# Kernel tuning notes

Hardware: AMD Instinct MI355X
Metric: run time of the kernel (lower is better)

The kernel has to match this reference:

```python
import jax, jax.numpy as jnp
import numpy as np

B, S, D, H = 2, 2048, 1024, 16  # batch, seq_len, model dim, heads


def setup_inputs() -> dict:
    key = jax.random.key(0)
    ks = jax.random.split(key, 5)
    return {
        "x": jax.random.normal(ks[0], (B, S, D), jnp.float32),
        "idx": jax.random.randint(ks[1], (B,), 0, S),
        "weight": jnp.float32(0.5),
        "attn_forcing": 1,  # static python flag
        "w_qkv": jax.random.normal(ks[2], (D, 3 * D), jnp.float32) * 0.02,
        "b_qkv": jnp.zeros((3 * D,), jnp.float32),
        "w_proj": jax.random.normal(ks[3], (D, D), jnp.float32) * 0.02,
        "b_proj": jnp.zeros((D,), jnp.float32),
    }


def reference(x, idx, weight, attn_forcing, w_qkv, b_qkv, w_proj, b_proj):
    Bx, Sx, Dm = x.shape
    dh = Dm // H
    # qkv projection (Conv1D: x @ w + b)
    qkv = x @ w_qkv + b_qkv  # [B,S,3D]
    q, k, v = jnp.split(qkv, 3, axis=-1)
    q = q.reshape(Bx, Sx, H, dh).transpose(0, 2, 1, 3)  # [B,H,S,dh]
    k = k.reshape(Bx, Sx, H, dh).transpose(0, 2, 1, 3)
    v = v.reshape(Bx, Sx, H, dh).transpose(0, 2, 1, 3)
    alen = jnp.arange(Sx)
    mask = (alen[None, :] <= alen[:, None]).astype(x.dtype)  # [S,S] causal
    w = jnp.einsum('bhqd,bhkd->bhqk', q, k) / jnp.asarray(np.sqrt(dh), x.dtype)
    w = w * mask + jnp.asarray(-1e9, x.dtype) * (1 - mask)
    w = jax.nn.softmax(w, axis=-1)
    if attn_forcing:
        # post-softmax forcing reweight: positions >= idx scaled by weight, then renorm
        a = jnp.where(alen[None, :] >= idx[:, None], weight, jnp.asarray(1.0, x.dtype))  # [B,S]
        w = w * a[:, None, None, :]
        w = w / jnp.sum(w, axis=-1, keepdims=True)
    out = jnp.einsum('bhqk,bhkd->bhqd', w, v)  # [B,H,S,dh]
    out = out.transpose(0, 2, 1, 3).reshape(Bx, Sx, Dm)  # merge heads
    return out @ w_proj + b_proj
```

## Files before the change

### kernel.cpp

```cpp
#include <hip/hip_runtime.h>


typedef __attribute__((ext_vector_type(8))) short short8;
typedef __attribute__((ext_vector_type(4))) float f32x4;

#define MFMA_B16(a, b, c) __builtin_amdgcn_mfma_f32_16x16x32_bf16(a, b, c, 0, 0, 0)

#if __has_builtin(__builtin_amdgcn_exp2f)
#define EXP2(x) __builtin_amdgcn_exp2f(x)
#else
#define EXP2(x) exp2f(x)
#endif

static __device__ __forceinline__ unsigned short f2bf(float f) {
    union { float f; unsigned int u; } v;
    v.f = f;
    unsigned int r = (v.u + 0x7fffu + ((v.u >> 16) & 1u)) >> 16;
    return (unsigned short)r;
}

static __device__ __forceinline__ unsigned int pk_bf16(float a, float b) {
#if __has_builtin(__builtin_amdgcn_cvt_pk_bf16_f32)
    typedef __bf16 bf2 __attribute__((ext_vector_type(2)));
    union { bf2 v; unsigned int u; } c;
    c.v = __builtin_amdgcn_cvt_pk_bf16_f32(a, b);
    return c.u;
#else
    return (unsigned int)f2bf(a) | ((unsigned int)f2bf(b) << 16);
#endif
}

static __device__ __forceinline__ void gl_lds16(const void* g, void* l) {
    __builtin_amdgcn_global_load_lds(
        (const __attribute__((address_space(1))) unsigned int*)g,
        (__attribute__((address_space(3))) unsigned int*)l, 16, 0, 0);
}

__global__ __launch_bounds__(256) void convert_x_kernel(const float4* __restrict__ x,
                                                        ushort4* __restrict__ xb) {
    int i = blockIdx.x * 256 + threadIdx.x;
    float4 v = x[i];
    ushort4 o;
    o.x = f2bf(v.x); o.y = f2bf(v.y); o.z = f2bf(v.z); o.w = f2bf(v.w);
    xb[i] = o;
}

__global__ __launch_bounds__(256) void transpose_cvt_kernel(const float* __restrict__ in,
                                                            unsigned short* __restrict__ out,
                                                            int R, int C) {
    __shared__ float t[32][33];
    int c0 = blockIdx.x * 32, r0 = blockIdx.y * 32;
    int x = threadIdx.x, y = threadIdx.y;
    #pragma unroll
    for (int yy = y; yy < 32; yy += 8)
        t[yy][x] = in[(size_t)(r0 + yy) * C + (c0 + x)];
    __syncthreads();
    #pragma unroll
    for (int yy = y; yy < 32; yy += 8)
        out[(size_t)(c0 + yy) * R + (r0 + x)] = f2bf(t[x][yy]);
}

__global__ __launch_bounds__(256) void gemm_qkv_kernel(const unsigned short* __restrict__ A,
                                                       const unsigned short* __restrict__ Bt,
                                                       const float* __restrict__ bias,
                                                       unsigned short* __restrict__ q,
                                                       unsigned short* __restrict__ k,
                                                       unsigned short* __restrict__ vT) {
    __shared__ unsigned short As[128 * 64];
    __shared__ unsigned short Bs[128 * 64];
    const int tid = threadIdx.x;
    const int lane = tid & 63, wave = tid >> 6;
    const int l15 = lane & 15, quad = lane >> 4;
    const int wm = wave >> 1, wn = wave & 1;
    const int row0 = blockIdx.y * 128, col0 = blockIdx.x * 128;
    const int K = 1024;

    int srow[4], scol[4], sdst[4];
    #pragma unroll
    for (int h = 0; h < 4; ++h) {
        int D = h * 256 + wave * 64 + lane;
        srow[h] = D >> 3;
        scol[h] = ((D & 7) ^ (srow[h] & 7)) * 8;
        sdst[h] = (h * 256 + wave * 64) * 8;
    }

    f32x4 acc[4][4] = {};

    for (int kt = 0; kt < K; kt += 64) {
        #pragma unroll
        for (int h = 0; h < 4; ++h) {
            gl_lds16(&A[(size_t)(row0 + srow[h]) * K + kt + scol[h]], &As[sdst[h]]);
            gl_lds16(&Bt[(size_t)(col0 + srow[h]) * K + kt + scol[h]], &Bs[sdst[h]]);
        }
        __syncthreads();
        #pragma unroll
        for (int kk = 0; kk < 2; ++kk) {
            short8 af[4], bf[4];
            #pragma unroll
            for (int i = 0; i < 4; ++i) {
                int r = wm * 64 + i * 16 + l15;
                af[i] = *(const short8*)&As[r * 64 + (((kk * 4 + quad) ^ (r & 7)) * 8)];
            }
            #pragma unroll
            for (int j = 0; j < 4; ++j) {
                int r = wn * 64 + j * 16 + l15;
                bf[j] = *(const short8*)&Bs[r * 64 + (((kk * 4 + quad) ^ (r & 7)) * 8)];
            }
            #pragma unroll
            for (int i = 0; i < 4; ++i)
                #pragma unroll
                for (int j = 0; j < 4; ++j)
                    acc[i][j] = MFMA_B16(af[i], bf[j], acc[i][j]);
        }
        __syncthreads();
    }

    const int b = row0 >> 11;
    const int srow0 = row0 & 2047;

    if (blockIdx.x < 16) {
        #pragma unroll
        for (int i = 0; i < 4; ++i)
            #pragma unroll
            for (int j = 0; j < 4; ++j)
                #pragma unroll
                for (int r = 0; r < 4; ++r) {
                    int row = row0 + wm * 64 + i * 16 + quad * 4 + r;
                    int col = col0 + wn * 64 + j * 16 + l15;
                    float val = acc[i][j][r] + bias[col];
                    int which = col >> 10, rem = col & 1023;
                    int hh = rem >> 6, d = rem & 63;
                    int s = row & 2047;
                    size_t o = ((size_t)((b * 16 + hh) * 2048 + s)) * 64 + d;
                    if (which == 0) q[o] = f2bf(val * 0.1803368867f);
                    else k[o] = f2bf(val);
                }
    } else {
        unsigned short* tb = (wn == 0) ? As : Bs;
        #pragma unroll
        for (int i = 0; i < 4; ++i)
            #pragma unroll
            for (int j = 0; j < 4; ++j) {
                const int col6 = j * 16 + l15;
                const int gcol = col0 + wn * 64 + col6;
                const float bb = bias[gcol];
                const int chunk = wm * 8 + i * 2 + (quad >> 1);
                unsigned int* pw = (unsigned int*)&tb[col6 * 128 +
                    ((chunk ^ (col6 & 15)) * 8) + (quad & 1) * 4];
                pw[0] = pk_bf16(acc[i][j][0] + bb, acc[i][j][1] + bb);
                pw[1] = pk_bf16(acc[i][j][2] + bb, acc[i][j][3] + bb);
            }
        __syncthreads();
        const int c = tid >> 1;
        const int half = c >> 6, col6 = c & 63;
        const int rhalf = (tid & 1) * 64;
        const unsigned short* src = half ? Bs : As;
        const int hh = (blockIdx.x - 16) * 2 + half;
        unsigned short* dst = vT + ((size_t)((b * 16 + hh) * 64 + col6)) * 2048 + srow0 + rhalf;
        #pragma unroll
        for (int kk = 0; kk < 8; ++kk) {
            const int chunk = ((rhalf >> 3) + kk) ^ (col6 & 15);
            *(short8*)&dst[kk * 8] = *(const short8*)&src[col6 * 128 + chunk * 8];
        }
    }
}

__global__ __launch_bounds__(256) void gemm_proj_kernel(const unsigned short* __restrict__ A,
                                                        const unsigned short* __restrict__ Bt,
                                                        const float* __restrict__ bias,
                                                        float* __restrict__ out) {
    __shared__ unsigned short As[128 * 64];
    __shared__ unsigned short Bs[64 * 64];
    const int tid = threadIdx.x;
    const int lane = tid & 63, wave = tid >> 6;
    const int l15 = lane & 15, quad = lane >> 4;
    const int wm = wave >> 1, wn = wave & 1;
    const int row0 = blockIdx.y * 128, col0 = blockIdx.x * 64;
    const int K = 1024;

    int srow[4], scol[4], sdst[4];
    #pragma unroll
    for (int h = 0; h < 4; ++h) {
        int D = h * 256 + wave * 64 + lane;
        srow[h] = D >> 3;
        scol[h] = ((D & 7) ^ (srow[h] & 7)) * 8;
        sdst[h] = (h * 256 + wave * 64) * 8;
    }

    f32x4 acc[4][2] = {};

    for (int kt = 0; kt < K; kt += 64) {
        #pragma unroll
        for (int h = 0; h < 4; ++h)
            gl_lds16(&A[(size_t)(row0 + srow[h]) * K + kt + scol[h]], &As[sdst[h]]);
        #pragma unroll
        for (int h = 0; h < 2; ++h)
            gl_lds16(&Bt[(size_t)(col0 + srow[h]) * K + kt + scol[h]], &Bs[sdst[h]]);
        __syncthreads();
        #pragma unroll
        for (int kk = 0; kk < 2; ++kk) {
            short8 af[4], bf[2];
            #pragma unroll
            for (int i = 0; i < 4; ++i) {
                int r = wm * 64 + i * 16 + l15;
                af[i] = *(const short8*)&As[r * 64 + (((kk * 4 + quad) ^ (r & 7)) * 8)];
            }
            #pragma unroll
            for (int j = 0; j < 2; ++j) {
                int r = wn * 32 + j * 16 + l15;
                bf[j] = *(const short8*)&Bs[r * 64 + (((kk * 4 + quad) ^ (r & 7)) * 8)];
            }
            #pragma unroll
            for (int i = 0; i < 4; ++i)
                #pragma unroll
                for (int j = 0; j < 2; ++j)
                    acc[i][j] = MFMA_B16(af[i], bf[j], acc[i][j]);
        }
        __syncthreads();
    }

    #pragma unroll
    for (int i = 0; i < 4; ++i)
        #pragma unroll
        for (int j = 0; j < 2; ++j)
            #pragma unroll
            for (int r = 0; r < 4; ++r) {
                int row = row0 + wm * 64 + i * 16 + quad * 4 + r;
                int col = col0 + wn * 32 + j * 16 + l15;
                out[(size_t)row * 1024 + col] = acc[i][j][r] + bias[col];
            }
}

__global__ __launch_bounds__(256) void attn_kernel(const unsigned short* __restrict__ Q,
                                                   const unsigned short* __restrict__ Kg,
                                                   const unsigned short* __restrict__ Vt,
                                                   const int* __restrict__ idx,
                                                   const float* __restrict__ weight,
                                                   const int* __restrict__ forcing,
                                                   unsigned short* __restrict__ O) {
    __shared__ unsigned short Ks[2][4096];
    __shared__ unsigned short Vs[2][4096];
    __shared__ unsigned short Pw[4][1024];

    const int tid = threadIdx.x;
    const int lane = tid & 63, wave = tid >> 6;
    const int l15 = lane & 15, quad = lane >> 4;
    const int bid = blockIdx.x;
    const int u = bid >> 5, a = u & 7, qg = u >> 3;
    const int t = (qg == 0) ? (31 - a) : (qg == 1) ? (16 + a) : (qg == 2) ? (15 - a) : a;
    const int bh = bid & 31;
    const int b = bh >> 4, hh = bh & 15;
    const unsigned short* Qb = Q + (size_t)bh * 2048 * 64;
    const unsigned short* Kh = Kg + (size_t)bh * 2048 * 64;
    const unsigned short* Vh = Vt + (size_t)bh * 2048 * 64;

    const int idxb = idx[b];
    const float lw = (forcing[0] != 0) ? __log2f(weight[0]) : 0.0f;

    const int L0 = wave * 128 + lane;
    const int rS = L0 >> 3;
    const int cS = (L0 & 7) ^ (rS & 7);
    const int ldsOffJ0 = (wave * 128) * 8;
    const int ldsOffJ1 = (wave * 128 + 64) * 8;

    const int q0 = t * 64 + wave * 16;
    const int qrow = q0 + l15;

    short8 aq0 = *(const short8*)&Qb[(q0 + l15) * 64 + quad * 8];
    short8 aq1 = *(const short8*)&Qb[(q0 + l15) * 64 + 32 + quad * 8];

    const short8 ones8 = {0x3F80, 0x3F80, 0x3F80, 0x3F80, 0x3F80, 0x3F80, 0x3F80, 0x3F80};

    f32x4 o[4] = {};
    f32x4 lsum = {};

    const int nkb = t + 1;

    {
        const unsigned short* kg = Kh + (size_t)rS * 64 + cS * 8;
        const unsigned short* vg = Vh + (size_t)rS * 2048 + cS * 8;
        gl_lds16(kg,            &Ks[0][ldsOffJ0]);
        gl_lds16(kg + 8 * 64,   &Ks[0][ldsOffJ1]);
        gl_lds16(vg,            &Vs[0][ldsOffJ0]);
        gl_lds16(vg + 8 * 2048, &Vs[0][ldsOffJ1]);
    }
    __syncthreads();

    unsigned short* const pwb = &Pw[wave][0];
    const int pwr = l15 * 64;
    const int pa7 = l15 & 7;

    for (int kb = 0; kb < nkb; ++kb) {
        const int cur = kb & 1;
        const int kbase = kb * 64;
        if (kb + 1 < nkb) {
            const int nb = kbase + 64;
            const unsigned short* kg = Kh + (size_t)(nb + rS) * 64 + cS * 8;
            const unsigned short* vg = Vh + (size_t)rS * 2048 + nb + cS * 8;
            gl_lds16(kg,            &Ks[cur ^ 1][ldsOffJ0]);
            gl_lds16(kg + 8 * 64,   &Ks[cur ^ 1][ldsOffJ1]);
            gl_lds16(vg,            &Vs[cur ^ 1][ldsOffJ0]);
            gl_lds16(vg + 8 * 2048, &Vs[cur ^ 1][ldsOffJ1]);
        }

        const bool fullF = (kbase >= idxb);
        const bool bndF = (!fullF) && (kbase + 63 >= idxb);
        const float zu = fullF ? lw : 0.0f;

        f32x4 sT[4];
        #pragma unroll
        for (int kt = 0; kt < 4; ++kt) {
            const int row = kt * 16 + l15;
            short8 k0 = *(const short8*)&Ks[cur][row * 64 + ((quad ^ (row & 7)) * 8)];
            short8 k1 = *(const short8*)&Ks[cur][row * 64 + (((4 + quad) ^ (row & 7)) * 8)];
            f32x4 z;
            if (!bndF) {
                z[0] = zu; z[1] = zu; z[2] = zu; z[3] = zu;
            } else {
                #pragma unroll
                for (int r = 0; r < 4; ++r)
                    z[r] = (kbase + kt * 16 + quad * 4 + r >= idxb) ? lw : 0.0f;
            }
            z = MFMA_B16(k0, aq0, z);
            z = MFMA_B16(k1, aq1, z);
            sT[kt] = z;
        }

        if (kb == t) {
            #pragma unroll
            for (int kt = 0; kt < 4; ++kt)
                #pragma unroll
                for (int r = 0; r < 4; ++r)
                    if (kbase + kt * 16 + quad * 4 + r > qrow) sT[kt][r] = -3.0e38f;
        }

        #pragma unroll
        for (int kt = 0; kt < 4; ++kt)
            #pragma unroll
            for (int r = 0; r < 4; ++r)
                sT[kt][r] = EXP2(sT[kt][r]);

        #pragma unroll
        for (int kt = 0; kt < 4; ++kt) {
            unsigned int* pw = (unsigned int*)&pwb[pwr +
                (((kt * 2 + (quad >> 1)) ^ pa7) * 8) + (quad & 1) * 4];
            pw[0] = pk_bf16(sT[kt][0], sT[kt][1]);
            pw[1] = pk_bf16(sT[kt][2], sT[kt][3]);
        }

        short8 bp0 = *(const short8*)&pwb[pwr + ((quad ^ pa7) * 8)];
        short8 bp1 = *(const short8*)&pwb[pwr + (((4 + quad) ^ pa7) * 8)];

        lsum = MFMA_B16(ones8, bp0, lsum);
        lsum = MFMA_B16(ones8, bp1, lsum);

        #pragma unroll
        for (int dt = 0; dt < 4; ++dt) {
            const int row = dt * 16 + l15;
            short8 vf0 = *(const short8*)&Vs[cur][row * 64 + ((quad ^ (row & 7)) * 8)];
            short8 vf1 = *(const short8*)&Vs[cur][row * 64 + (((4 + quad) ^ (row & 7)) * 8)];
            f32x4 oo = o[dt];
            oo = MFMA_B16(vf0, bp0, oo);
            oo = MFMA_B16(vf1, bp1, oo);
            o[dt] = oo;
        }

        __syncthreads();
    }

    const float inv = 1.0f / lsum[0];
    unsigned short* sc = &Ks[0][0] + wave * 1152;
    #pragma unroll
    for (int dt = 0; dt < 4; ++dt)
        #pragma unroll
        for (int r = 0; r < 4; ++r)
            sc[l15 * 72 + dt * 16 + quad * 4 + r] = f2bf(o[dt][r] * inv);
    const size_t rowoff = ((size_t)(b * 2048 + q0 + l15)) * 1024 + hh * 64;
    #pragma unroll
    for (int h = 0; h < 2; ++h) {
        short8 v8 = *(const short8*)&sc[l15 * 72 + quad * 16 + h * 8];
        *(short8*)&O[rowoff + quad * 16 + h * 8] = v8;
    }
}

extern "C" void kernel_launch(void* const* d_in, const int* in_sizes, int n_in,
                              void* d_out, int out_size, void* d_ws, size_t ws_size,
                              hipStream_t stream) {
    const float* x        = (const float*)d_in[0];
    const int*   idx      = (const int*)d_in[1];
    const float* weight   = (const float*)d_in[2];
    const int*   forcing  = (const int*)d_in[3];
    const float* w_qkv    = (const float*)d_in[4];
    const float* b_qkv    = (const float*)d_in[5];
    const float* w_proj   = (const float*)d_in[6];
    const float* b_proj   = (const float*)d_in[7];
    float* out = (float*)d_out;

    char* ws = (char*)d_ws;
    unsigned short* xb      = (unsigned short*)(ws);
    unsigned short* wqkvT   = (unsigned short*)(ws + 8388608);
    unsigned short* wprojT  = (unsigned short*)(ws + 14680064);
    unsigned short* qbuf    = (unsigned short*)(ws + 16777216);
    unsigned short* kbuf    = (unsigned short*)(ws + 25165824);
    unsigned short* vTbuf   = (unsigned short*)(ws + 33554432);
    unsigned short* attn_out = xb;

    convert_x_kernel<<<4096, 256, 0, stream>>>((const float4*)x, (ushort4*)xb);
    transpose_cvt_kernel<<<dim3(96, 32), dim3(32, 8), 0, stream>>>(w_qkv, wqkvT, 1024, 3072);
    transpose_cvt_kernel<<<dim3(32, 32), dim3(32, 8), 0, stream>>>(w_proj, wprojT, 1024, 1024);
    gemm_qkv_kernel<<<dim3(24, 32), 256, 0, stream>>>(xb, wqkvT, b_qkv, qbuf, kbuf, vTbuf);
    attn_kernel<<<1024, 256, 0, stream>>>(qbuf, kbuf, vTbuf, idx, weight, forcing, attn_out);
    gemm_proj_kernel<<<dim3(16, 32), 256, 0, stream>>>(attn_out, wprojT, b_proj, out);
}
```

Measured before the change: 194.3 us.

## Merge prep kernels and swap MFMA operands for vectorized GEMM epilogues

Merges the x conversion and the two weight transpose-convert launches into one prep kernel. Swaps the MFMA operand order in the Q/K and projection GEMMs so each lane holds four consecutive output columns, which lets the epilogues write packed bf16 uint2 and float4 stores instead of scalar ones. The V epilogue no longer goes through an LDS transpose and writes transposed rows straight from registers. This trims launch overhead and uncoalesced scalar stores, but the direct V stores are 8-byte pieces that may coalesce less well than the old LDS-staged 16-byte writes.

Result: faster. 189.4 us (-2.5%).

```diff
diff --git a/kernel.cpp b/kernel.cpp
--- a/kernel.cpp
+++ b/kernel.cpp
@@ -36,28 +36,43 @@
         (__attribute__((address_space(3))) unsigned int*)l, 16, 0, 0);
 }
 
-__global__ __launch_bounds__(256) void convert_x_kernel(const float4* __restrict__ x,
-                                                        ushort4* __restrict__ xb) {
-    int i = blockIdx.x * 256 + threadIdx.x;
-    float4 v = x[i];
-    ushort4 o;
-    o.x = f2bf(v.x); o.y = f2bf(v.y); o.z = f2bf(v.z); o.w = f2bf(v.w);
-    xb[i] = o;
-}
-
-__global__ __launch_bounds__(256) void transpose_cvt_kernel(const float* __restrict__ in,
-                                                            unsigned short* __restrict__ out,
-                                                            int R, int C) {
+__global__ __launch_bounds__(256) void prep_kernel(const float4* __restrict__ x,
+                                                   ushort4* __restrict__ xb,
+                                                   const float* __restrict__ wqkv,
+                                                   unsigned short* __restrict__ wqkvT,
+                                                   const float* __restrict__ wproj,
+                                                   unsigned short* __restrict__ wprojT) {
+    const int bid = blockIdx.x;
+    if (bid < 4096) {
+        int i = bid * 256 + threadIdx.x;
+        float4 v = x[i];
+        ushort4 o;
+        o.x = f2bf(v.x); o.y = f2bf(v.y); o.z = f2bf(v.z); o.w = f2bf(v.w);
+        xb[i] = o;
+        return;
+    }
     __shared__ float t[32][33];
-    int c0 = blockIdx.x * 32, r0 = blockIdx.y * 32;
-    int x = threadIdx.x, y = threadIdx.y;
-    #pragma unroll
-    for (int yy = y; yy < 32; yy += 8)
-        t[yy][x] = in[(size_t)(r0 + yy) * C + (c0 + x)];
+    const float* in;
+    unsigned short* out;
+    int R, C, bx, by;
+    if (bid < 4096 + 3072) {
+        int g = bid - 4096;
+        in = wqkv; out = wqkvT; R = 1024; C = 3072;
+        bx = g % 96; by = g / 96;
+    } else {
+        int g = bid - 7168;
+        in = wproj; out = wprojT; R = 1024; C = 1024;
+        bx = g & 31; by = g >> 5;
+    }
+    const int c0 = bx * 32, r0 = by * 32;
+    const int xx = threadIdx.x & 31, yy0 = threadIdx.x >> 5;
+    #pragma unroll
+    for (int yy = yy0; yy < 32; yy += 8)
+        t[yy][xx] = in[(size_t)(r0 + yy) * C + (c0 + xx)];
     __syncthreads();
     #pragma unroll
-    for (int yy = y; yy < 32; yy += 8)
-        out[(size_t)(c0 + yy) * R + (r0 + x)] = f2bf(t[x][yy]);
+    for (int yy = yy0; yy < 32; yy += 8)
+        out[(size_t)(c0 + yy) * R + (r0 + xx)] = f2bf(t[xx][yy]);
 }
 
 __global__ __launch_bounds__(256) void gemm_qkv_kernel(const unsigned short* __restrict__ A,
@@ -74,6 +89,7 @@
     const int wm = wave >> 1, wn = wave & 1;
     const int row0 = blockIdx.y * 128, col0 = blockIdx.x * 128;
     const int K = 1024;
+    const bool isV = (blockIdx.x >= 16);
 
     int srow[4], scol[4], sdst[4];
     #pragma unroll
@@ -106,61 +122,59 @@
                 int r = wn * 64 + j * 16 + l15;
                 bf[j] = *(const short8*)&Bs[r * 64 + (((kk * 4 + quad) ^ (r & 7)) * 8)];
             }
-            #pragma unroll
-            for (int i = 0; i < 4; ++i)
+            if (isV) {
                 #pragma unroll
-                for (int j = 0; j < 4; ++j)
-                    acc[i][j] = MFMA_B16(af[i], bf[j], acc[i][j]);
+                for (int i = 0; i < 4; ++i)
+                    #pragma unroll
+                    for (int j = 0; j < 4; ++j)
+                        acc[i][j] = MFMA_B16(af[i], bf[j], acc[i][j]);
+            } else {
+                #pragma unroll
+                for (int i = 0; i < 4; ++i)
+                    #pragma unroll
+                    for (int j = 0; j < 4; ++j)
+                        acc[i][j] = MFMA_B16(bf[j], af[i], acc[i][j]);
+            }
         }
         __syncthreads();
     }
 
     const int b = row0 >> 11;
-    const int srow0 = row0 & 2047;
-
-    if (blockIdx.x < 16) {
-        #pragma unroll
-        for (int i = 0; i < 4; ++i)
-            #pragma unroll
-            for (int j = 0; j < 4; ++j)
-                #pragma unroll
-                for (int r = 0; r < 4; ++r) {
-                    int row = row0 + wm * 64 + i * 16 + quad * 4 + r;
-                    int col = col0 + wn * 64 + j * 16 + l15;
-                    float val = acc[i][j][r] + bias[col];
-                    int which = col >> 10, rem = col & 1023;
-                    int hh = rem >> 6, d = rem & 63;
-                    int s = row & 2047;
-                    size_t o = ((size_t)((b * 16 + hh) * 2048 + s)) * 64 + d;
-                    if (which == 0) q[o] = f2bf(val * 0.1803368867f);
-                    else k[o] = f2bf(val);
-                }
+    const int s0 = row0 & 2047;
+    const float* bb = bias + col0 + wn * 64;
+
+    if (!isV) {
+        const int which = blockIdx.x >> 3;
+        unsigned short* dst = which ? k : q;
+        const float scale = which ? 1.0f : 0.1803368867f;
+        const int hh = ((blockIdx.x & 7) << 1) + wn;
+        #pragma unroll
+        for (int i = 0; i < 4; ++i) {
+            const int s = s0 + wm * 64 + i * 16 + l15;
+            unsigned short* drow = dst + ((size_t)((b * 16 + hh) * 2048 + s)) * 64;
+            #pragma unroll
+            for (int j = 0; j < 4; ++j) {
+                float4 b4 = ((const float4*)bb)[j * 4 + quad];
+                uint2 pv;
+                pv.x = pk_bf16((acc[i][j][0] + b4.x) * scale, (acc[i][j][1] + b4.y) * scale);
+                pv.y = pk_bf16((acc[i][j][2] + b4.z) * scale, (acc[i][j][3] + b4.w) * scale);
+                *(uint2*)&drow[j * 16 + quad * 4] = pv;
+            }
+        }
     } else {
-        unsigned short* tb = (wn == 0) ? As : Bs;
-        #pragma unroll
-        for (int i = 0; i < 4; ++i)
-            #pragma unroll
-            for (int j = 0; j < 4; ++j) {
-                const int col6 = j * 16 + l15;
-                const int gcol = col0 + wn * 64 + col6;
-                const float bb = bias[gcol];
-                const int chunk = wm * 8 + i * 2 + (quad >> 1);
-                unsigned int* pw = (unsigned int*)&tb[col6 * 128 +
-                    ((chunk ^ (col6 & 15)) * 8) + (quad & 1) * 4];
-                pw[0] = pk_bf16(acc[i][j][0] + bb, acc[i][j][1] + bb);
-                pw[1] = pk_bf16(acc[i][j][2] + bb, acc[i][j][3] + bb);
-            }
-        __syncthreads();
-        const int c = tid >> 1;
-        const int half = c >> 6, col6 = c & 63;
-        const int rhalf = (tid & 1) * 64;
-        const unsigned short* src = half ? Bs : As;
-        const int hh = (blockIdx.x - 16) * 2 + half;
-        unsigned short* dst = vT + ((size_t)((b * 16 + hh) * 64 + col6)) * 2048 + srow0 + rhalf;
-        #pragma unroll
-        for (int kk = 0; kk < 8; ++kk) {
-            const int chunk = ((rhalf >> 3) + kk) ^ (col6 & 15);
-            *(short8*)&dst[kk * 8] = *(const short8*)&src[col6 * 128 + chunk * 8];
+        const int hh = ((blockIdx.x - 16) << 1) + wn;
+        #pragma unroll
+        for (int j = 0; j < 4; ++j) {
+            const int d = j * 16 + l15;
+            const float bv = bb[d];
+            unsigned short* drow = vT + ((size_t)((b * 16 + hh) * 64 + d)) * 2048 + s0;
+            #pragma unroll
+            for (int i = 0; i < 4; ++i) {
+                uint2 pv;
+                pv.x = pk_bf16(acc[i][j][0] + bv, acc[i][j][1] + bv);
+                pv.y = pk_bf16(acc[i][j][2] + bv, acc[i][j][3] + bv);
+                *(uint2*)&drow[wm * 64 + i * 16 + quad * 4] = pv;
+            }
         }
     }
 }
@@ -214,21 +228,26 @@
             for (int i = 0; i < 4; ++i)
                 #pragma unroll
                 for (int j = 0; j < 2; ++j)
-                    acc[i][j] = MFMA_B16(af[i], bf[j], acc[i][j]);
+                    acc[i][j] = MFMA_B16(bf[j], af[i], acc[i][j]);
         }
         __syncthreads();
     }
 
-    #pragma unroll
-    for (int i = 0; i < 4; ++i)
-        #pragma unroll
-        for (int j = 0; j < 2; ++j)
-            #pragma unroll
-            for (int r = 0; r < 4; ++r) {
-                int row = row0 + wm * 64 + i * 16 + quad * 4 + r;
-                int col = col0 + wn * 32 + j * 16 + l15;
-                out[(size_t)row * 1024 + col] = acc[i][j][r] + bias[col];
-            }
+    const float* bb = bias + col0 + wn * 32;
+    #pragma unroll
+    for (int i = 0; i < 4; ++i) {
+        const int row = row0 + wm * 64 + i * 16 + l15;
+        #pragma unroll
+        for (int j = 0; j < 2; ++j) {
+            float4 b4 = ((const float4*)bb)[j * 4 + quad];
+            float4 ov;
+            ov.x = acc[i][j][0] + b4.x;
+            ov.y = acc[i][j][1] + b4.y;
+            ov.z = acc[i][j][2] + b4.z;
+            ov.w = acc[i][j][3] + b4.w;
+            *(float4*)&out[(size_t)row * 1024 + col0 + wn * 32 + j * 16 + quad * 4] = ov;
+        }
+    }
 }
 
 __global__ __launch_bounds__(256) void attn_kernel(const unsigned short* __restrict__ Q,
@@ -405,9 +424,8 @@
     unsigned short* vTbuf   = (unsigned short*)(ws + 33554432);
     unsigned short* attn_out = xb;
 
-    convert_x_kernel<<<4096, 256, 0, stream>>>((const float4*)x, (ushort4*)xb);
-    transpose_cvt_kernel<<<dim3(96, 32), dim3(32, 8), 0, stream>>>(w_qkv, wqkvT, 1024, 3072);
-    transpose_cvt_kernel<<<dim3(32, 32), dim3(32, 8), 0, stream>>>(w_proj, wprojT, 1024, 1024);
+    prep_kernel<<<8192, 256, 0, stream>>>((const float4*)x, (ushort4*)xb,
+                                          w_qkv, wqkvT, w_proj, wprojT);
     gemm_qkv_kernel<<<dim3(24, 32), 256, 0, stream>>>(xb, wqkvT, b_qkv, qbuf, kbuf, vTbuf);
     attn_kernel<<<1024, 256, 0, stream>>>(qbuf, kbuf, vTbuf, idx, weight, forcing, attn_out);
     gemm_proj_kernel<<<dim3(16, 32), 256, 0, stream>>>(attn_out, wprojT, b_proj, out);
```
